# Kernel tuning notes

Measured on AMD Instinct MI355X. Metric: run time of the kernel, lower is better.

## Reference

```python
import jax, jax.numpy as jnp
import numpy as np

H = 512      # hidden_dim
K = 3        # conv_kernel_size
CHUNK = 3    # chunk_size
EPS = 1e-5   # BatchNorm eps


def conv1d(x, w, b, pad):
    # x: (B, Cin, L), w: (Cout, Cin, K)
    y = jax.lax.conv_general_dilated(x, w, (1,), [(pad, pad)],
                                     dimension_numbers=("NCH", "OIH", "NCH"))
    return y + b[None, :, None]


def chunk_indices(seq_lens):
    # static int metadata -> numpy index build (loop over small fixed batch only)
    sl = np.asarray(seq_lens)
    bidx, sidx = [], []
    for b, l in enumerate(sl):
        starts = np.arange(0, int(l) - CHUNK + 1, CHUNK)
        bidx.append(np.full(starts.shape[0], b, dtype=np.int32))
        sidx.append(starts.astype(np.int32))
    return np.concatenate(bidx), np.concatenate(sidx)


def setup_inputs() -> dict:
    key = jax.random.key(0)
    ks = jax.random.split(key, 8)
    B, L = 32, 4096
    x = jax.random.normal(ks[0], (B, L), jnp.float32)
    seq_lens = jax.random.randint(ks[1], (B,), 2048, L + 1)

    def w(k, shape):
        return jax.random.normal(k, shape, jnp.float32) * 0.05

    return {
        "x": x,
        "w0": w(ks[2], (H, 1, K)), "b0": jnp.zeros((H,)), "g0": jnp.ones((H,)), "be0": jnp.zeros((H,)),
        "w1": w(ks[3], (H, H, K)), "b1": jnp.zeros((H,)), "g1": jnp.ones((H,)), "be1": jnp.zeros((H,)),
        "w2": w(ks[4], (H, H, K)), "b2": jnp.zeros((H,)), "g2": jnp.ones((H,)), "be2": jnp.zeros((H,)),
        "pw": w(ks[5], (H, H, CHUNK)), "pb": jnp.zeros((H,)),
        "fw": w(ks[6], (1, H)), "fb": jnp.zeros((1,)),
        "seq_lens": seq_lens,
    }


def reference(x, w0, b0, g0, be0, w1, b1, g1, be1, w2, b2, g2, be2,
              pw, pb, fw, fb, seq_lens):
    inv = np.float32(1.0 / np.sqrt(1.0 + EPS))  # BN eval: mean=0, var=1
    h = x[:, None, :]  # (B, 1, L)
    for (w, b, g, be) in ((w0, b0, g0, be0), (w1, b1, g1, be1), (w2, b2, g2, be2)):
        h = jax.nn.relu(conv1d(h, w, b, pad=1))
        h = (g * inv)[None, :, None] * h + be[None, :, None]
    h = jnp.transpose(h, (0, 2, 1))  # (B, L, H)

    bidx_np, sidx_np = chunk_indices(seq_lens)
    bidx = jnp.asarray(bidx_np)
    sidx = jnp.asarray(sidx_np)
    offs = jnp.arange(CHUNK, dtype=jnp.int32)
    chunks = h[bidx[:, None], sidx[:, None] + offs[None, :], :]  # (N, CHUNK, H)

    # pre_fc_conv over a length-CHUNK window == one GEMM per chunk
    z = jnp.einsum("nth,cht->nc", chunks, pw) + pb  # (N, H)
    logits = jax.nn.relu(z) @ fw.T + fb             # (N, 1)
    return jax.nn.sigmoid(logits)[:, 0]             # (N,)
```

## Files before the change

kernel.cpp:

```cpp
#include <hip/hip_runtime.h>

#define HCH 512
#define LSEQ 4096
#define HSTR (LSEQ + 4)
#define NB 32
#define KW 3
#define KDIM 1536
#define INVS 0.9999950000374997f
#define NT 24

typedef __attribute__((ext_vector_type(8))) short bf16x8;
typedef __attribute__((ext_vector_type(4))) float f32x4;

__device__ inline unsigned short f2bf(float f) {
  unsigned int u = __float_as_uint(f);
  u += 0x7fffu + ((u >> 16) & 1u);
  return (unsigned short)(u >> 16);
}

__device__ inline void gl_lds16(const void* g, void* l) {
  __builtin_amdgcn_global_load_lds(
      (const __attribute__((address_space(1))) void*)g,
      (__attribute__((address_space(3))) void*)l, 16, 0, 0);
}

__global__ void prep_all(const float* __restrict__ w1, const float* __restrict__ w2,
                         const float* __restrict__ pw, unsigned short* __restrict__ wt,
                         const int* __restrict__ seq_lens, int* __restrict__ cum,
                         float* __restrict__ pz, int nz,
                         unsigned short* __restrict__ hbuf, int nbp) {
  int idx = blockIdx.x * 256 + threadIdx.x;
  if (idx < nz) pz[idx] = 0.f;
  if (idx == 0) {
    int acc = 0;
    for (int b = 0; b < NB; b++) {
      cum[b] = acc;
      acc += (seq_lens[b] - KW) / KW + 1;
    }
  }
  int npads = 2 * nbp * 4 * HCH;
  if (idx < npads) {
    int per = nbp * 4 * HCH;
    int buf = idx / per, r = idx % per;
    int b = r / (4 * HCH), rr = r % (4 * HCH);
    int j = rr / HCH, c = rr % HCH;
    int row = (j == 0) ? 0 : (LSEQ + j);
    hbuf[((size_t)buf * nbp + b) * HSTR * HCH + (size_t)row * HCH + c] = 0;
  }
  if (idx < 3 * HCH * KDIM) {
    int which = idx / (HCH * KDIM);
    int r = idx % (HCH * KDIM);
    int c = r / KDIM;
    int rem = r % KDIM;
    int k = rem / HCH, ci = rem % HCH;
    const float* src = (which == 0) ? w1 : ((which == 1) ? w2 : pw);
    wt[idx] = f2bf(src[c * KDIM + ci * KW + k]);
  }
}

__global__ void layer0(const float* __restrict__ x, const float* __restrict__ w0,
                       const float* __restrict__ b0, const float* __restrict__ g0,
                       const float* __restrict__ be0, unsigned short* __restrict__ h0,
                       const int* __restrict__ seq_q) {
  int tid = threadIdx.x;
  int wave = tid >> 6, lane = tid & 63;
  int pos0 = (blockIdx.x * 4 + wave) * 8;
  int l0 = pos0 & (LSEQ - 1);
  int bq = pos0 >> 12;
  if (l0 >= seq_q[bq] + 2) return;
  int c0 = lane * 8;

  float w[24], bb[8], gg[8], ee[8];
  for (int v = 0; v < 6; v++)
    *reinterpret_cast<float4*>(w + v * 4) = *reinterpret_cast<const float4*>(w0 + c0 * 3 + v * 4);
  for (int v = 0; v < 2; v++) {
    *reinterpret_cast<float4*>(bb + v * 4) = *reinterpret_cast<const float4*>(b0 + c0 + v * 4);
    *reinterpret_cast<float4*>(gg + v * 4) = *reinterpret_cast<const float4*>(g0 + c0 + v * 4);
    *reinterpret_cast<float4*>(ee + v * 4) = *reinterpret_cast<const float4*>(be0 + c0 + v * 4);
  }
  for (int c = 0; c < 8; c++) gg[c] *= INVS;

  const float* xb = x + (size_t)(pos0 - l0);
  unsigned short* hrow = h0 + ((size_t)bq * HSTR + 1 + l0) * HCH + c0;
  for (int pp = 0; pp < 8; pp++) {
    int l = l0 + pp;
    float xm1 = (l > 0) ? xb[l - 1] : 0.f;
    float xc = xb[l];
    float xp1 = (l < LSEQ - 1) ? xb[l + 1] : 0.f;
    unsigned int o[4];
    for (int pq = 0; pq < 4; pq++) {
      unsigned int lo = 0, hi = 0;
      for (int s = 0; s < 2; s++) {
        int c = pq * 2 + s;
        float y = w[c * 3] * xm1 + w[c * 3 + 1] * xc + w[c * 3 + 2] * xp1 + bb[c];
        y = fmaxf(y, 0.f);
        unsigned int u = f2bf(gg[c] * y + ee[c]);
        if (s == 0) lo = u; else hi = u;
      }
      o[pq] = lo | (hi << 16);
    }
    uint4 v4; v4.x = o[0]; v4.y = o[1]; v4.z = o[2]; v4.w = o[3];
    *reinterpret_cast<uint4*>(hrow + (size_t)pp * HCH) = v4;
  }
}

#define OFFK(T) (((T) % 3) * HCH + ((T) / 3) * 64)

#define STAGE_A(Mh, AB, TN)                                                 \
  { char* d_ = ldsc + (AB) * 32768 + (Mh) * 16384 + w * 1024;               \
    gl_lds16(aSrc[Mh][0] + OFFK(TN), d_);                                   \
    gl_lds16(aSrc[Mh][1] + OFFK(TN), d_ + 8192); }

#define STAGE_B(Nh, BB, TN)                                                 \
  { char* d_ = ldsc + 65536 + (BB) * 32768 + (Nh) * 16384 + w * 1024;       \
    gl_lds16(bSrc[Nh][0] + OFFK(TN), d_);                                   \
    gl_lds16(bSrc[Nh][1] + OFFK(TN), d_ + 8192); }

#define LOAD_AF(Mh, AB)                                                     \
  _Pragma("unroll") for (int i_ = 0; i_ < 4; ++i_)                          \
  _Pragma("unroll") for (int s_ = 0; s_ < 2; ++s_)                          \
    af[i_][s_] = *reinterpret_cast<const bf16x8*>(                          \
        ldsb + (AB) * 16384 + (Mh) * 8192 + (wm + i_ * 16 + mr) * 64 +      \
        (((s_ * 4 + quad) ^ (mr & 7)) << 3));

#define LOAD_BF(Nh, BB)                                                     \
  _Pragma("unroll") for (int j_ = 0; j_ < 2; ++j_)                          \
  _Pragma("unroll") for (int s_ = 0; s_ < 2; ++s_)                          \
    bfv[Nh][j_][s_] = *reinterpret_cast<const bf16x8*>(                     \
        ldsb + 32768 + (BB) * 16384 + (Nh) * 8192 + (wn + j_ * 16 + mr) * 64 + \
        (((s_ * 4 + quad) ^ (mr & 7)) << 3));

#define MFMA_Q(MB, Nh)                                                      \
  __builtin_amdgcn_s_setprio(1);                                            \
  _Pragma("unroll") for (int i_ = 0; i_ < 4; ++i_)                          \
  _Pragma("unroll") for (int j_ = 0; j_ < 2; ++j_)                          \
  _Pragma("unroll") for (int s_ = 0; s_ < 2; ++s_)                          \
    acc[(MB) + i_][(Nh)*2 + j_] = __builtin_amdgcn_mfma_f32_16x16x32_bf16(  \
        af[i_][s_], bfv[Nh][j_][s_], acc[(MB) + i_][(Nh)*2 + j_], 0, 0, 0); \
  __builtin_amdgcn_s_setprio(0);

#define BARRIER { asm volatile("" ::: "memory");                            \
                  __builtin_amdgcn_s_barrier();                             \
                  asm volatile("" ::: "memory"); }
#define WAITV(n) asm volatile("s_waitcnt vmcnt(" #n ")" ::: "memory");

#define STEP(T)                                                             \
  {                                                                         \
    if ((T) == NT - 1) { WAITV(0); } else { WAITV(4); }                     \
    BARRIER;                                                                \
    if ((T) + 1 < NT) { STAGE_A(0, ((T)+1)&1, (T)+1);                       \
                        STAGE_A(1, ((T)+1)&1, (T)+1); }                     \
    if ((T) + 2 < NT) { STAGE_B(0, ((T)+2)%3, (T)+2);                       \
                        STAGE_B(1, ((T)+2)%3, (T)+2); }                     \
    bf16x8 af[4][2], bfv[2][2][2];                                          \
    LOAD_AF(0, (T)&1);                                                      \
    LOAD_BF(0, (T)%3); LOAD_BF(1, (T)%3);                                   \
    MFMA_Q(0, 0); MFMA_Q(0, 1);                                             \
    LOAD_AF(1, (T)&1);                                                      \
    MFMA_Q(4, 1); MFMA_Q(4, 0);                                             \
  }

__global__ __launch_bounds__(512, 2) void conv_gemm8(
    const unsigned short* __restrict__ hin,
    const unsigned short* __restrict__ wT,
    const float* __restrict__ bconv, const float* __restrict__ g,
    const float* __restrict__ be,
    unsigned short* __restrict__ hout,
    const int* __restrict__ seq_q, int margin) {
  __shared__ unsigned short ldsb[81920];

  int f = blockIdx.x;
  int cpx = gridDim.x >> 3;
  int s = (f & 7) * cpx + (f >> 3);
  int cm = (s & 1) << 8;
  int y = s >> 1;
  int b = y >> 4;
  int l0 = (y & 15) << 8;
  int limit = seq_q[b] + margin;
  if (l0 >= limit) return;

  const size_t hb = (size_t)b * HSTR * HCH + HCH;
  int tid = threadIdx.x;
  int w = tid >> 6, lane = tid & 63;
  int quad = lane >> 4, mr = lane & 15;
  int wm = (w >> 2) << 6;
  int wn = (w & 3) << 5;
  int srow = tid >> 3;
  int sslot8 = (((tid & 7) ^ (srow & 7)) << 3);

  const unsigned short* aSrc[2][2];
#pragma unroll
  for (int Mh = 0; Mh < 2; ++Mh)
#pragma unroll
    for (int g2 = 0; g2 < 2; ++g2)
      aSrc[Mh][g2] = wT + (size_t)(cm + Mh * 128 + g2 * 64 + srow) * KDIM + sslot8;
  const unsigned short* bSrc[2][2];
#pragma unroll
  for (int Nh = 0; Nh < 2; ++Nh)
#pragma unroll
    for (int g2 = 0; g2 < 2; ++g2)
      bSrc[Nh][g2] = hin + hb +
          (size_t)(l0 - 1 + Nh * 128 + g2 * 64 + srow) * HCH + sslot8;

  f32x4 acc[8][4] = {};
  char* ldsc = (char*)ldsb;

  STAGE_A(0, 0, 0); STAGE_A(1, 0, 0);
  STAGE_B(0, 0, 0); STAGE_B(1, 0, 0);
  STAGE_B(0, 1, 1); STAGE_B(1, 1, 1);

  STEP(0)  STEP(1)  STEP(2)  STEP(3)  STEP(4)  STEP(5)
  STEP(6)  STEP(7)  STEP(8)  STEP(9)  STEP(10) STEP(11)
  STEP(12) STEP(13) STEP(14) STEP(15) STEP(16) STEP(17)
  STEP(18) STEP(19) STEP(20) STEP(21) STEP(22) STEP(23)

#pragma unroll
  for (int ai = 0; ai < 8; ++ai) {
    int Mh = ai >> 2, i = ai & 3;
    int c = cm + Mh * 128 + wm + i * 16 + quad * 4;
    f32x4 bc = *reinterpret_cast<const f32x4*>(bconv + c);
    f32x4 gg = *reinterpret_cast<const f32x4*>(g + c);
    f32x4 bb = *reinterpret_cast<const f32x4*>(be + c);
#pragma unroll
    for (int aj = 0; aj < 4; ++aj) {
      int Nh = aj >> 1, j = aj & 1;
      int n = l0 + Nh * 128 + wn + j * 16 + (lane & 15);
      if (n >= limit) continue;
      unsigned long long pack = 0;
#pragma unroll
      for (int r = 0; r < 4; ++r) {
        float yv = acc[ai][aj][r] + bc[r];
        yv = fmaxf(yv, 0.f);
        unsigned long long u = f2bf(gg[r] * INVS * yv + bb[r]);
        pack |= u << (16 * r);
      }
      *reinterpret_cast<unsigned long long*>(hout + hb + (size_t)n * HCH + c) = pack;
    }
  }
}

__global__ __launch_bounds__(512, 2) void chunk_gemm8(
    const unsigned short* __restrict__ h2,
    const unsigned short* __restrict__ wT,
    const float* __restrict__ pb, const float* __restrict__ fw,
    const int* __restrict__ seq_q,
    const int* __restrict__ cum_q,
    float* __restrict__ partial,
    const unsigned short* __restrict__ zp) {
  __shared__ unsigned short ldsb[81920];

  int f = blockIdx.x;
  int cpx = gridDim.x >> 3;
  int s = (f & 7) * cpx + (f >> 3);
  int cm = (s & 1) << 8;
  int y = s >> 1;
  int b = y / 6;
  int s_base = (y % 6) << 8;
  int slen = seq_q[b];
  if (3 * s_base + KW > slen) return;

  const size_t hb = (size_t)b * HSTR * HCH + HCH;
  int tid = threadIdx.x;
  int w = tid >> 6, lane = tid & 63;
  int quad = lane >> 4, mr = lane & 15;
  int wm = (w >> 2) << 6;
  int wn = (w & 3) << 5;
  int srow = tid >> 3;
  int sslot8 = (((tid & 7) ^ (srow & 7)) << 3);

  const unsigned short* aSrc[2][2];
#pragma unroll
  for (int Mh = 0; Mh < 2; ++Mh)
#pragma unroll
    for (int g2 = 0; g2 < 2; ++g2)
      aSrc[Mh][g2] = wT + (size_t)(cm + Mh * 128 + g2 * 64 + srow) * KDIM + sslot8;
  const unsigned short* bSrc[2][2];
#pragma unroll
  for (int Nh = 0; Nh < 2; ++Nh)
#pragma unroll
    for (int g2 = 0; g2 < 2; ++g2) {
      int slot = s_base + Nh * 128 + g2 * 64 + srow;
      bSrc[Nh][g2] = (slot <= 1365)
          ? h2 + hb + (size_t)(3 * slot) * HCH + sslot8
          : zp + sslot8;
    }

  f32x4 acc[8][4] = {};
  char* ldsc = (char*)ldsb;

  STAGE_A(0, 0, 0); STAGE_A(1, 0, 0);
  STAGE_B(0, 0, 0); STAGE_B(1, 0, 0);
  STAGE_B(0, 1, 1); STAGE_B(1, 1, 1);

  STEP(0)  STEP(1)  STEP(2)  STEP(3)  STEP(4)  STEP(5)
  STEP(6)  STEP(7)  STEP(8)  STEP(9)  STEP(10) STEP(11)
  STEP(12) STEP(13) STEP(14) STEP(15) STEP(16) STEP(17)
  STEP(18) STEP(19) STEP(20) STEP(21) STEP(22) STEP(23)

  int nn = lane & 15;
#pragma unroll
  for (int aj = 0; aj < 4; ++aj) {
    int Nh = aj >> 1, jj = aj & 1;
    int sc = s_base + Nh * 128 + wn + jj * 16 + nn;
    float sacc = 0.f;
#pragma unroll
    for (int ai = 0; ai < 8; ++ai) {
      int Mh = ai >> 2, i = ai & 3;
      int c = cm + Mh * 128 + wm + i * 16 + quad * 4;
      f32x4 pbv = *reinterpret_cast<const f32x4*>(pb + c);
      f32x4 fwv = *reinterpret_cast<const f32x4*>(fw + c);
#pragma unroll
      for (int r = 0; r < 4; ++r) {
        float z = acc[ai][aj][r] + pbv[r];
        z = fmaxf(z, 0.f);
        sacc += z * fwv[r];
      }
    }
    sacc += __shfl_xor(sacc, 16, 64);
    sacc += __shfl_xor(sacc, 32, 64);
    if (quad == 0 && 3 * sc + KW <= slen)
      atomicAdd(partial + cum_q[b] + sc, sacc);
  }
}

__global__ void finalize(const float* __restrict__ partial, const float* __restrict__ fb,
                         float* __restrict__ out, int n) {
  int i = blockIdx.x * 256 + threadIdx.x;
  if (i < n) {
    float t = partial[i] + fb[0];
    out[i] = 1.f / (1.f + expf(-t));
  }
}

extern "C" void kernel_launch(void* const* d_in, const int* in_sizes, int n_in,
                              void* d_out, int out_size, void* d_ws, size_t ws_size,
                              hipStream_t stream) {
  (void)in_sizes; (void)n_in;
  const float* x   = (const float*)d_in[0];
  const float* w0  = (const float*)d_in[1];
  const float* b0  = (const float*)d_in[2];
  const float* g0  = (const float*)d_in[3];
  const float* be0 = (const float*)d_in[4];
  const float* w1  = (const float*)d_in[5];
  const float* b1  = (const float*)d_in[6];
  const float* g1  = (const float*)d_in[7];
  const float* be1 = (const float*)d_in[8];
  const float* w2  = (const float*)d_in[9];
  const float* b2  = (const float*)d_in[10];
  const float* g2  = (const float*)d_in[11];
  const float* be2 = (const float*)d_in[12];
  const float* pw  = (const float*)d_in[13];
  const float* pb  = (const float*)d_in[14];
  const float* fw  = (const float*)d_in[15];
  const float* fb  = (const float*)d_in[16];
  const int* seq_lens = (const int*)d_in[17];

  char* ws = (char*)d_ws;
  unsigned short* zeropage = (unsigned short*)ws;
  float* partial = (float*)(ws + 4096);
  size_t off = 4096 + (size_t)out_size * 4;
  off = (off + 255) & ~(size_t)255;
  int* cum = (int*)(ws + off);
  off += NB * 4;
  off = (off + 255) & ~(size_t)255;
  unsigned short* wt = (unsigned short*)(ws + off);
  off += (size_t)3 * HCH * KDIM * 2;
  off = (off + 255) & ~(size_t)255;
  size_t fixed = off;

  const size_t per_batch = (size_t)HSTR * HCH * 2;
  int nb_pass = NB;
  while (nb_pass > 1 && fixed + 2 * per_batch * (size_t)nb_pass > ws_size)
    nb_pass >>= 1;
  unsigned short* h0 = (unsigned short*)(ws + fixed);
  unsigned short* h1 = h0 + (size_t)nb_pass * HSTR * HCH;

  int nzero = 1024 + out_size;
  prep_all<<<(3 * HCH * KDIM) / 256, 256, 0, stream>>>(w1, w2, pw, wt, seq_lens, cum,
                                                       (float*)ws, nzero, h0, nb_pass);

  int npass = NB / nb_pass;
  for (int q = 0; q < npass; q++) {
    const float* xq = x + (size_t)q * nb_pass * LSEQ;
    const int* sq = seq_lens + q * nb_pass;
    int nwg = nb_pass * 32;
    layer0<<<nb_pass * (LSEQ / 32), 256, 0, stream>>>(xq, w0, b0, g0, be0, h0, sq);
    conv_gemm8<<<nwg, 512, 0, stream>>>(h0, wt, b1, g1, be1, h1, sq, 1);
    conv_gemm8<<<nwg, 512, 0, stream>>>(h1, wt + (size_t)HCH * KDIM, b2, g2, be2, h0,
                                        sq, 0);
    int nwg2 = nb_pass * 12;
    chunk_gemm8<<<nwg2, 512, 0, stream>>>(h0, wt + (size_t)2 * HCH * KDIM, pb, fw,
                                          sq, cum + q * nb_pass, partial, zeropage);
  }
  finalize<<<(out_size + 255) / 256, 256, 0, stream>>>(partial, fb, (float*)d_out, out_size);
}
```

Measured before the change: 556.4 us.

## Reuse one staged activation window across the three conv taps

The conv GEMM now stages a single 320-row activation window (258 rows used, the rest padded from a zero page) per 64-channel slice into LDS. It reads all three tap offsets from that window by shifting the row index, where before it reloaded shifted B tiles for each tap. This cuts global-to-LDS traffic for the activation operand to roughly a third. In exchange the pipeline is reshaped: B staging is spread over three steps with double buffering by channel slice, and the vmcnt waits change, which may expose load latency at slice boundaries.

```diff
diff --git a/kernel.cpp b/kernel.cpp
--- a/kernel.cpp
+++ b/kernel.cpp
@@ -104,30 +104,23 @@
   }
 }
 
+#define BARRIER { asm volatile("" ::: "memory");                            \
+                  __builtin_amdgcn_s_barrier();                             \
+                  asm volatile("" ::: "memory"); }
+#define WAITV(n) asm volatile("s_waitcnt vmcnt(" #n ")" ::: "memory");
+
 #define OFFK(T) (((T) % 3) * HCH + ((T) / 3) * 64)
 
 #define STAGE_A(Mh, AB, TN)                                                 \
   { char* d_ = ldsc + (AB) * 32768 + (Mh) * 16384 + w * 1024;               \
     gl_lds16(aSrc[Mh][0] + OFFK(TN), d_);                                   \
     gl_lds16(aSrc[Mh][1] + OFFK(TN), d_ + 8192); }
-
-#define STAGE_B(Nh, BB, TN)                                                 \
-  { char* d_ = ldsc + 65536 + (BB) * 32768 + (Nh) * 16384 + w * 1024;       \
-    gl_lds16(bSrc[Nh][0] + OFFK(TN), d_);                                   \
-    gl_lds16(bSrc[Nh][1] + OFFK(TN), d_ + 8192); }
 
 #define LOAD_AF(Mh, AB)                                                     \
   _Pragma("unroll") for (int i_ = 0; i_ < 4; ++i_)                          \
   _Pragma("unroll") for (int s_ = 0; s_ < 2; ++s_)                          \
     af[i_][s_] = *reinterpret_cast<const bf16x8*>(                          \
         ldsb + (AB) * 16384 + (Mh) * 8192 + (wm + i_ * 16 + mr) * 64 +      \
-        (((s_ * 4 + quad) ^ (mr & 7)) << 3));
-
-#define LOAD_BF(Nh, BB)                                                     \
-  _Pragma("unroll") for (int j_ = 0; j_ < 2; ++j_)                          \
-  _Pragma("unroll") for (int s_ = 0; s_ < 2; ++s_)                          \
-    bfv[Nh][j_][s_] = *reinterpret_cast<const bf16x8*>(                     \
-        ldsb + 32768 + (BB) * 16384 + (Nh) * 8192 + (wn + j_ * 16 + mr) * 64 + \
         (((s_ * 4 + quad) ^ (mr & 7)) << 3));
 
 #define MFMA_Q(MB, Nh)                                                      \
@@ -139,10 +132,128 @@
         af[i_][s_], bfv[Nh][j_][s_], acc[(MB) + i_][(Nh)*2 + j_], 0, 0, 0); \
   __builtin_amdgcn_s_setprio(0);
 
-#define BARRIER { asm volatile("" ::: "memory");                            \
-                  __builtin_amdgcn_s_barrier();                             \
-                  asm volatile("" ::: "memory"); }
-#define WAITV(n) asm volatile("s_waitcnt vmcnt(" #n ")" ::: "memory");
+#define STAGE_BS(PB, S)                                                     \
+  gl_lds16(bSw[S] + (PB) * 64,                                              \
+           ldsc + 65536 + ((PB) & 1) * 40960 + (S) * 8192 + w * 1024);
+
+#define LOAD_BFD(Nh, CB, K)                                                 \
+  _Pragma("unroll") for (int j_ = 0; j_ < 2; ++j_)                          \
+  _Pragma("unroll") for (int s_ = 0; s_ < 2; ++s_) {                        \
+    int r_ = (Nh) * 128 + wn + j_ * 16 + mr + (K);                          \
+    bfv[Nh][j_][s_] = *reinterpret_cast<const bf16x8*>(                     \
+        ldsb + 32768 + (CB) * 20480 + r_ * 64 +                             \
+        (((s_ * 4 + quad) ^ (r_ & 7)) << 3)); }
+
+#define STEPD(T)                                                            \
+  {                                                                         \
+    if ((T) % 3 == 0 || (T) >= 21) { WAITV(0); } else { WAITV(2); }         \
+    BARRIER;                                                                \
+    if ((T) + 1 < NT) { STAGE_A(0, ((T)+1)&1, (T)+1);                       \
+                        STAGE_A(1, ((T)+1)&1, (T)+1); }                     \
+    if ((T) / 3 + 1 < 8) {                                                  \
+      if ((T) % 3 == 0) { STAGE_BS((T)/3 + 1, 0); STAGE_BS((T)/3 + 1, 1); } \
+      if ((T) % 3 == 1) { STAGE_BS((T)/3 + 1, 2); STAGE_BS((T)/3 + 1, 3); } \
+      if ((T) % 3 == 2) { STAGE_BS((T)/3 + 1, 4); }                         \
+    }                                                                       \
+    bf16x8 af[4][2], bfv[2][2][2];                                          \
+    LOAD_AF(0, (T)&1);                                                      \
+    LOAD_BFD(0, ((T)/3)&1, (T)%3); LOAD_BFD(1, ((T)/3)&1, (T)%3);           \
+    MFMA_Q(0, 0); MFMA_Q(0, 1);                                             \
+    LOAD_AF(1, (T)&1);                                                      \
+    MFMA_Q(4, 1); MFMA_Q(4, 0);                                             \
+  }
+
+__global__ __launch_bounds__(512, 2) void conv_gemmd(
+    const unsigned short* __restrict__ hin,
+    const unsigned short* __restrict__ wT,
+    const float* __restrict__ bconv, const float* __restrict__ g,
+    const float* __restrict__ be,
+    unsigned short* __restrict__ hout,
+    const unsigned short* __restrict__ zp,
+    const int* __restrict__ seq_q, int margin) {
+  __shared__ unsigned short ldsb[73728];
+
+  int f = blockIdx.x;
+  int cpx = gridDim.x >> 3;
+  int s = (f & 7) * cpx + (f >> 3);
+  int cm = (s & 1) << 8;
+  int y = s >> 1;
+  int b = y >> 4;
+  int l0 = (y & 15) << 8;
+  int limit = seq_q[b] + margin;
+  if (l0 >= limit) return;
+
+  const size_t hb = (size_t)b * HSTR * HCH + HCH;
+  int tid = threadIdx.x;
+  int w = tid >> 6, lane = tid & 63;
+  int quad = lane >> 4, mr = lane & 15;
+  int wm = (w >> 2) << 6;
+  int wn = (w & 3) << 5;
+  int srow = tid >> 3;
+  int sslot8 = (((tid & 7) ^ (srow & 7)) << 3);
+
+  const unsigned short* aSrc[2][2];
+#pragma unroll
+  for (int Mh = 0; Mh < 2; ++Mh)
+#pragma unroll
+    for (int g2 = 0; g2 < 2; ++g2)
+      aSrc[Mh][g2] = wT + (size_t)(cm + Mh * 128 + g2 * 64 + srow) * KDIM + sslot8;
+
+  const unsigned short* bSw[5];
+#pragma unroll
+  for (int sw = 0; sw < 5; ++sw) {
+    int r = sw * 64 + srow;
+    bSw[sw] = (r <= 258) ? hin + hb + (size_t)(l0 - 1 + r) * HCH + sslot8
+                         : zp + sslot8;
+  }
+
+  f32x4 acc[8][4] = {};
+  char* ldsc = (char*)ldsb;
+
+  STAGE_A(0, 0, 0); STAGE_A(1, 0, 0);
+  STAGE_BS(0, 0); STAGE_BS(0, 1); STAGE_BS(0, 2); STAGE_BS(0, 3); STAGE_BS(0, 4);
+
+  STEPD(0)  STEPD(1)  STEPD(2)  STEPD(3)  STEPD(4)  STEPD(5)
+  STEPD(6)  STEPD(7)  STEPD(8)  STEPD(9)  STEPD(10) STEPD(11)
+  STEPD(12) STEPD(13) STEPD(14) STEPD(15) STEPD(16) STEPD(17)
+  STEPD(18) STEPD(19) STEPD(20) STEPD(21) STEPD(22) STEPD(23)
+
+#pragma unroll
+  for (int ai = 0; ai < 8; ++ai) {
+    int Mh = ai >> 2, i = ai & 3;
+    int c = cm + Mh * 128 + wm + i * 16 + quad * 4;
+    f32x4 bc = *reinterpret_cast<const f32x4*>(bconv + c);
+    f32x4 gg = *reinterpret_cast<const f32x4*>(g + c);
+    f32x4 bb = *reinterpret_cast<const f32x4*>(be + c);
+#pragma unroll
+    for (int aj = 0; aj < 4; ++aj) {
+      int Nh = aj >> 1, j = aj & 1;
+      int n = l0 + Nh * 128 + wn + j * 16 + (lane & 15);
+      if (n >= limit) continue;
+      unsigned long long pack = 0;
+#pragma unroll
+      for (int r = 0; r < 4; ++r) {
+        float yv = acc[ai][aj][r] + bc[r];
+        yv = fmaxf(yv, 0.f);
+        unsigned long long u = f2bf(gg[r] * INVS * yv + bb[r]);
+        pack |= u << (16 * r);
+      }
+      *reinterpret_cast<unsigned long long*>(hout + hb + (size_t)n * HCH + c) = pack;
+    }
+  }
+}
+
+#define STAGE_B(Nh, BB, TN)                                                 \
+  { char* d_ = ldsc + 65536 + (BB) * 32768 + (Nh) * 16384 + w * 1024;       \
+    gl_lds16(bSrc[Nh][0] + OFFK(TN), d_);                                   \
+    gl_lds16(bSrc[Nh][1] + OFFK(TN), d_ + 8192); }
+
+#define LOAD_BF(Nh, BB)                                                     \
+  _Pragma("unroll") for (int j_ = 0; j_ < 2; ++j_)                          \
+  _Pragma("unroll") for (int s_ = 0; s_ < 2; ++s_)                          \
+    bfv[Nh][j_][s_] = *reinterpret_cast<const bf16x8*>(                     \
+        ldsb + 32768 + (BB) * 16384 + (Nh) * 8192 + (wn + j_ * 16 + mr) * 64 + \
+        (((s_ * 4 + quad) ^ (mr & 7)) << 3));
 
 #define STEP(T)                                                             \
   {                                                                         \
@@ -159,85 +270,6 @@
     LOAD_AF(1, (T)&1);                                                      \
     MFMA_Q(4, 1); MFMA_Q(4, 0);                                             \
   }
-
-__global__ __launch_bounds__(512, 2) void conv_gemm8(
-    const unsigned short* __restrict__ hin,
-    const unsigned short* __restrict__ wT,
-    const float* __restrict__ bconv, const float* __restrict__ g,
-    const float* __restrict__ be,
-    unsigned short* __restrict__ hout,
-    const int* __restrict__ seq_q, int margin) {
-  __shared__ unsigned short ldsb[81920];
-
-  int f = blockIdx.x;
-  int cpx = gridDim.x >> 3;
-  int s = (f & 7) * cpx + (f >> 3);
-  int cm = (s & 1) << 8;
-  int y = s >> 1;
-  int b = y >> 4;
-  int l0 = (y & 15) << 8;
-  int limit = seq_q[b] + margin;
-  if (l0 >= limit) return;
-
-  const size_t hb = (size_t)b * HSTR * HCH + HCH;
-  int tid = threadIdx.x;
-  int w = tid >> 6, lane = tid & 63;
-  int quad = lane >> 4, mr = lane & 15;
-  int wm = (w >> 2) << 6;
-  int wn = (w & 3) << 5;
-  int srow = tid >> 3;
-  int sslot8 = (((tid & 7) ^ (srow & 7)) << 3);
-
-  const unsigned short* aSrc[2][2];
-#pragma unroll
-  for (int Mh = 0; Mh < 2; ++Mh)
-#pragma unroll
-    for (int g2 = 0; g2 < 2; ++g2)
-      aSrc[Mh][g2] = wT + (size_t)(cm + Mh * 128 + g2 * 64 + srow) * KDIM + sslot8;
-  const unsigned short* bSrc[2][2];
-#pragma unroll
-  for (int Nh = 0; Nh < 2; ++Nh)
-#pragma unroll
-    for (int g2 = 0; g2 < 2; ++g2)
-      bSrc[Nh][g2] = hin + hb +
-          (size_t)(l0 - 1 + Nh * 128 + g2 * 64 + srow) * HCH + sslot8;
-
-  f32x4 acc[8][4] = {};
-  char* ldsc = (char*)ldsb;
-
-  STAGE_A(0, 0, 0); STAGE_A(1, 0, 0);
-  STAGE_B(0, 0, 0); STAGE_B(1, 0, 0);
-  STAGE_B(0, 1, 1); STAGE_B(1, 1, 1);
-
-  STEP(0)  STEP(1)  STEP(2)  STEP(3)  STEP(4)  STEP(5)
-  STEP(6)  STEP(7)  STEP(8)  STEP(9)  STEP(10) STEP(11)
-  STEP(12) STEP(13) STEP(14) STEP(15) STEP(16) STEP(17)
-  STEP(18) STEP(19) STEP(20) STEP(21) STEP(22) STEP(23)
-
-#pragma unroll
-  for (int ai = 0; ai < 8; ++ai) {
-    int Mh = ai >> 2, i = ai & 3;
-    int c = cm + Mh * 128 + wm + i * 16 + quad * 4;
-    f32x4 bc = *reinterpret_cast<const f32x4*>(bconv + c);
-    f32x4 gg = *reinterpret_cast<const f32x4*>(g + c);
-    f32x4 bb = *reinterpret_cast<const f32x4*>(be + c);
-#pragma unroll
-    for (int aj = 0; aj < 4; ++aj) {
-      int Nh = aj >> 1, j = aj & 1;
-      int n = l0 + Nh * 128 + wn + j * 16 + (lane & 15);
-      if (n >= limit) continue;
-      unsigned long long pack = 0;
-#pragma unroll
-      for (int r = 0; r < 4; ++r) {
-        float yv = acc[ai][aj][r] + bc[r];
-        yv = fmaxf(yv, 0.f);
-        unsigned long long u = f2bf(gg[r] * INVS * yv + bb[r]);
-        pack |= u << (16 * r);
-      }
-      *reinterpret_cast<unsigned long long*>(hout + hb + (size_t)n * HCH + c) = pack;
-    }
-  }
-}
 
 __global__ __launch_bounds__(512, 2) void chunk_gemm8(
     const unsigned short* __restrict__ h2,
@@ -385,9 +417,9 @@
     const int* sq = seq_lens + q * nb_pass;
     int nwg = nb_pass * 32;
     layer0<<<nb_pass * (LSEQ / 32), 256, 0, stream>>>(xq, w0, b0, g0, be0, h0, sq);
-    conv_gemm8<<<nwg, 512, 0, stream>>>(h0, wt, b1, g1, be1, h1, sq, 1);
-    conv_gemm8<<<nwg, 512, 0, stream>>>(h1, wt + (size_t)HCH * KDIM, b2, g2, be2, h0,
-                                        sq, 0);
+    conv_gemmd<<<nwg, 512, 0, stream>>>(h0, wt, b1, g1, be1, h1, zeropage, sq, 1);
+    conv_gemmd<<<nwg, 512, 0, stream>>>(h1, wt + (size_t)HCH * KDIM, b2, g2, be2, h0,
+                                        zeropage, sq, 0);
     int nwg2 = nb_pass * 12;
     chunk_gemm8<<<nwg2, 512, 0, stream>>>(h0, wt + (size_t)2 * HCH * KDIM, pb, fw,
                                           sq, cum + q * nb_pass, partial, zeropage);
```

Measured after the change: 563.5 us. About the same (+1.3%).

## Load weight fragments directly from global memory in conv GEMM, stage only activations

Applied to the files above, without the earlier changes.

Replaces the conv-layer GEMM with a variant that reads the A (weight) MFMA fragments straight from global memory into registers instead of staging them through LDS. Only the activation tile is staged via global_load_lds into a triple buffer, which shrinks LDS from 160KB to 96KB per block, and the barrier and wait placement is reordered. The goal is to cut LDS traffic and staging instructions and ease occupancy limits. The cost is that weight loads now go through the cache with strided per-lane access and their latency sits on the MFMA critical path.

```diff
diff --git a/kernel.cpp b/kernel.cpp
--- a/kernel.cpp
+++ b/kernel.cpp
@@ -104,31 +104,12 @@
   }
 }
 
+#define BARRIER { asm volatile("" ::: "memory");                            \
+                  __builtin_amdgcn_s_barrier();                             \
+                  asm volatile("" ::: "memory"); }
+#define WAITV(n) asm volatile("s_waitcnt vmcnt(" #n ")" ::: "memory");
+
 #define OFFK(T) (((T) % 3) * HCH + ((T) / 3) * 64)
-
-#define STAGE_A(Mh, AB, TN)                                                 \
-  { char* d_ = ldsc + (AB) * 32768 + (Mh) * 16384 + w * 1024;               \
-    gl_lds16(aSrc[Mh][0] + OFFK(TN), d_);                                   \
-    gl_lds16(aSrc[Mh][1] + OFFK(TN), d_ + 8192); }
-
-#define STAGE_B(Nh, BB, TN)                                                 \
-  { char* d_ = ldsc + 65536 + (BB) * 32768 + (Nh) * 16384 + w * 1024;       \
-    gl_lds16(bSrc[Nh][0] + OFFK(TN), d_);                                   \
-    gl_lds16(bSrc[Nh][1] + OFFK(TN), d_ + 8192); }
-
-#define LOAD_AF(Mh, AB)                                                     \
-  _Pragma("unroll") for (int i_ = 0; i_ < 4; ++i_)                          \
-  _Pragma("unroll") for (int s_ = 0; s_ < 2; ++s_)                          \
-    af[i_][s_] = *reinterpret_cast<const bf16x8*>(                          \
-        ldsb + (AB) * 16384 + (Mh) * 8192 + (wm + i_ * 16 + mr) * 64 +      \
-        (((s_ * 4 + quad) ^ (mr & 7)) << 3));
-
-#define LOAD_BF(Nh, BB)                                                     \
-  _Pragma("unroll") for (int j_ = 0; j_ < 2; ++j_)                          \
-  _Pragma("unroll") for (int s_ = 0; s_ < 2; ++s_)                          \
-    bfv[Nh][j_][s_] = *reinterpret_cast<const bf16x8*>(                     \
-        ldsb + 32768 + (BB) * 16384 + (Nh) * 8192 + (wn + j_ * 16 + mr) * 64 + \
-        (((s_ * 4 + quad) ^ (mr & 7)) << 3));
 
 #define MFMA_Q(MB, Nh)                                                      \
   __builtin_amdgcn_s_setprio(1);                                            \
@@ -139,10 +120,141 @@
         af[i_][s_], bfv[Nh][j_][s_], acc[(MB) + i_][(Nh)*2 + j_], 0, 0, 0); \
   __builtin_amdgcn_s_setprio(0);
 
-#define BARRIER { asm volatile("" ::: "memory");                            \
-                  __builtin_amdgcn_s_barrier();                             \
-                  asm volatile("" ::: "memory"); }
-#define WAITV(n) asm volatile("s_waitcnt vmcnt(" #n ")" ::: "memory");
+#define LOAD_AG(Mh, T)                                                      \
+  _Pragma("unroll") for (int i_ = 0; i_ < 4; ++i_)                          \
+  _Pragma("unroll") for (int s_ = 0; s_ < 2; ++s_)                          \
+    af[i_][s_] = *reinterpret_cast<const bf16x8*>(                          \
+        aP[Mh][i_] + OFFK(T) + s_ * 32);
+
+#define STAGE_B2(Nh, BB, TN)                                                \
+  { char* d_ = ldsc + (BB) * 32768 + (Nh) * 16384 + w * 1024;               \
+    gl_lds16(bSrc[Nh][0] + OFFK(TN), d_);                                   \
+    gl_lds16(bSrc[Nh][1] + OFFK(TN), d_ + 8192); }
+
+#define LOAD_BF2(Nh, BB)                                                    \
+  _Pragma("unroll") for (int j_ = 0; j_ < 2; ++j_)                          \
+  _Pragma("unroll") for (int s_ = 0; s_ < 2; ++s_)                          \
+    bfv[Nh][j_][s_] = *reinterpret_cast<const bf16x8*>(                     \
+        ldsb + (BB) * 16384 + (Nh) * 8192 + (wn + j_ * 16 + mr) * 64 +      \
+        (((s_ * 4 + quad) ^ (mr & 7)) << 3));
+
+#define STEPL(T)                                                            \
+  {                                                                         \
+    BARRIER;                                                                \
+    bf16x8 af[4][2], bfv[2][2][2];                                          \
+    LOAD_AG(0, T);                                                          \
+    LOAD_BF2(0, (T) % 3); LOAD_BF2(1, (T) % 3);                             \
+    MFMA_Q(0, 0); MFMA_Q(0, 1);                                             \
+    LOAD_AG(1, T);                                                          \
+    if ((T) + 2 < NT) { STAGE_B2(0, ((T)+2)%3, (T)+2);                      \
+                        STAGE_B2(1, ((T)+2)%3, (T)+2); }                    \
+    MFMA_Q(4, 1); MFMA_Q(4, 0);                                             \
+    if ((T) + 2 < NT) { WAITV(4); } else { WAITV(0); }                      \
+  }
+
+__global__ __launch_bounds__(512, 2) void conv_gemmA(
+    const unsigned short* __restrict__ hin,
+    const unsigned short* __restrict__ wT,
+    const float* __restrict__ bconv, const float* __restrict__ g,
+    const float* __restrict__ be,
+    unsigned short* __restrict__ hout,
+    const int* __restrict__ seq_q, int margin) {
+  __shared__ unsigned short ldsb[49152];
+
+  int f = blockIdx.x;
+  int cpx = gridDim.x >> 3;
+  int s = (f & 7) * cpx + (f >> 3);
+  int cm = (s & 1) << 8;
+  int y = s >> 1;
+  int b = y >> 4;
+  int l0 = (y & 15) << 8;
+  int limit = seq_q[b] + margin;
+  if (l0 >= limit) return;
+
+  const size_t hb = (size_t)b * HSTR * HCH + HCH;
+  int tid = threadIdx.x;
+  int w = tid >> 6, lane = tid & 63;
+  int quad = lane >> 4, mr = lane & 15;
+  int wm = (w >> 2) << 6;
+  int wn = (w & 3) << 5;
+  int srow = tid >> 3;
+  int sslot8 = (((tid & 7) ^ (srow & 7)) << 3);
+
+  const unsigned short* aP[2][4];
+#pragma unroll
+  for (int Mh = 0; Mh < 2; ++Mh)
+#pragma unroll
+    for (int i = 0; i < 4; ++i)
+      aP[Mh][i] = wT + (size_t)(cm + Mh * 128 + wm + i * 16 + mr) * KDIM + quad * 8;
+
+  const unsigned short* bSrc[2][2];
+#pragma unroll
+  for (int Nh = 0; Nh < 2; ++Nh)
+#pragma unroll
+    for (int g2 = 0; g2 < 2; ++g2)
+      bSrc[Nh][g2] = hin + hb +
+          (size_t)(l0 - 1 + Nh * 128 + g2 * 64 + srow) * HCH + sslot8;
+
+  f32x4 acc[8][4] = {};
+  char* ldsc = (char*)ldsb;
+
+  STAGE_B2(0, 0, 0); STAGE_B2(1, 0, 0);
+  WAITV(0);
+  STAGE_B2(0, 1, 1); STAGE_B2(1, 1, 1);
+
+  STEPL(0)  STEPL(1)  STEPL(2)  STEPL(3)  STEPL(4)  STEPL(5)
+  STEPL(6)  STEPL(7)  STEPL(8)  STEPL(9)  STEPL(10) STEPL(11)
+  STEPL(12) STEPL(13) STEPL(14) STEPL(15) STEPL(16) STEPL(17)
+  STEPL(18) STEPL(19) STEPL(20) STEPL(21) STEPL(22) STEPL(23)
+
+#pragma unroll
+  for (int ai = 0; ai < 8; ++ai) {
+    int Mh = ai >> 2, i = ai & 3;
+    int c = cm + Mh * 128 + wm + i * 16 + quad * 4;
+    f32x4 bc = *reinterpret_cast<const f32x4*>(bconv + c);
+    f32x4 gg = *reinterpret_cast<const f32x4*>(g + c);
+    f32x4 bb = *reinterpret_cast<const f32x4*>(be + c);
+#pragma unroll
+    for (int aj = 0; aj < 4; ++aj) {
+      int Nh = aj >> 1, j = aj & 1;
+      int n = l0 + Nh * 128 + wn + j * 16 + (lane & 15);
+      if (n >= limit) continue;
+      unsigned long long pack = 0;
+#pragma unroll
+      for (int r = 0; r < 4; ++r) {
+        float yv = acc[ai][aj][r] + bc[r];
+        yv = fmaxf(yv, 0.f);
+        unsigned long long u = f2bf(gg[r] * INVS * yv + bb[r]);
+        pack |= u << (16 * r);
+      }
+      *reinterpret_cast<unsigned long long*>(hout + hb + (size_t)n * HCH + c) = pack;
+    }
+  }
+}
+
+#define STAGE_A(Mh, AB, TN)                                                 \
+  { char* d_ = ldsc + (AB) * 32768 + (Mh) * 16384 + w * 1024;               \
+    gl_lds16(aSrc[Mh][0] + OFFK(TN), d_);                                   \
+    gl_lds16(aSrc[Mh][1] + OFFK(TN), d_ + 8192); }
+
+#define STAGE_B(Nh, BB, TN)                                                 \
+  { char* d_ = ldsc + 65536 + (BB) * 32768 + (Nh) * 16384 + w * 1024;       \
+    gl_lds16(bSrc[Nh][0] + OFFK(TN), d_);                                   \
+    gl_lds16(bSrc[Nh][1] + OFFK(TN), d_ + 8192); }
+
+#define LOAD_AF(Mh, AB)                                                     \
+  _Pragma("unroll") for (int i_ = 0; i_ < 4; ++i_)                          \
+  _Pragma("unroll") for (int s_ = 0; s_ < 2; ++s_)                          \
+    af[i_][s_] = *reinterpret_cast<const bf16x8*>(                          \
+        ldsb + (AB) * 16384 + (Mh) * 8192 + (wm + i_ * 16 + mr) * 64 +      \
+        (((s_ * 4 + quad) ^ (mr & 7)) << 3));
+
+#define LOAD_BF(Nh, BB)                                                     \
+  _Pragma("unroll") for (int j_ = 0; j_ < 2; ++j_)                          \
+  _Pragma("unroll") for (int s_ = 0; s_ < 2; ++s_)                          \
+    bfv[Nh][j_][s_] = *reinterpret_cast<const bf16x8*>(                     \
+        ldsb + 32768 + (BB) * 16384 + (Nh) * 8192 + (wn + j_ * 16 + mr) * 64 + \
+        (((s_ * 4 + quad) ^ (mr & 7)) << 3));
 
 #define STEP(T)                                                             \
   {                                                                         \
@@ -159,85 +271,6 @@
     LOAD_AF(1, (T)&1);                                                      \
     MFMA_Q(4, 1); MFMA_Q(4, 0);                                             \
   }
-
-__global__ __launch_bounds__(512, 2) void conv_gemm8(
-    const unsigned short* __restrict__ hin,
-    const unsigned short* __restrict__ wT,
-    const float* __restrict__ bconv, const float* __restrict__ g,
-    const float* __restrict__ be,
-    unsigned short* __restrict__ hout,
-    const int* __restrict__ seq_q, int margin) {
-  __shared__ unsigned short ldsb[81920];
-
-  int f = blockIdx.x;
-  int cpx = gridDim.x >> 3;
-  int s = (f & 7) * cpx + (f >> 3);
-  int cm = (s & 1) << 8;
-  int y = s >> 1;
-  int b = y >> 4;
-  int l0 = (y & 15) << 8;
-  int limit = seq_q[b] + margin;
-  if (l0 >= limit) return;
-
-  const size_t hb = (size_t)b * HSTR * HCH + HCH;
-  int tid = threadIdx.x;
-  int w = tid >> 6, lane = tid & 63;
-  int quad = lane >> 4, mr = lane & 15;
-  int wm = (w >> 2) << 6;
-  int wn = (w & 3) << 5;
-  int srow = tid >> 3;
-  int sslot8 = (((tid & 7) ^ (srow & 7)) << 3);
-
-  const unsigned short* aSrc[2][2];
-#pragma unroll
-  for (int Mh = 0; Mh < 2; ++Mh)
-#pragma unroll
-    for (int g2 = 0; g2 < 2; ++g2)
-      aSrc[Mh][g2] = wT + (size_t)(cm + Mh * 128 + g2 * 64 + srow) * KDIM + sslot8;
-  const unsigned short* bSrc[2][2];
-#pragma unroll
-  for (int Nh = 0; Nh < 2; ++Nh)
-#pragma unroll
-    for (int g2 = 0; g2 < 2; ++g2)
-      bSrc[Nh][g2] = hin + hb +
-          (size_t)(l0 - 1 + Nh * 128 + g2 * 64 + srow) * HCH + sslot8;
-
-  f32x4 acc[8][4] = {};
-  char* ldsc = (char*)ldsb;
-
-  STAGE_A(0, 0, 0); STAGE_A(1, 0, 0);
-  STAGE_B(0, 0, 0); STAGE_B(1, 0, 0);
-  STAGE_B(0, 1, 1); STAGE_B(1, 1, 1);
-
-  STEP(0)  STEP(1)  STEP(2)  STEP(3)  STEP(4)  STEP(5)
-  STEP(6)  STEP(7)  STEP(8)  STEP(9)  STEP(10) STEP(11)
-  STEP(12) STEP(13) STEP(14) STEP(15) STEP(16) STEP(17)
-  STEP(18) STEP(19) STEP(20) STEP(21) STEP(22) STEP(23)
-
-#pragma unroll
-  for (int ai = 0; ai < 8; ++ai) {
-    int Mh = ai >> 2, i = ai & 3;
-    int c = cm + Mh * 128 + wm + i * 16 + quad * 4;
-    f32x4 bc = *reinterpret_cast<const f32x4*>(bconv + c);
-    f32x4 gg = *reinterpret_cast<const f32x4*>(g + c);
-    f32x4 bb = *reinterpret_cast<const f32x4*>(be + c);
-#pragma unroll
-    for (int aj = 0; aj < 4; ++aj) {
-      int Nh = aj >> 1, j = aj & 1;
-      int n = l0 + Nh * 128 + wn + j * 16 + (lane & 15);
-      if (n >= limit) continue;
-      unsigned long long pack = 0;
-#pragma unroll
-      for (int r = 0; r < 4; ++r) {
-        float yv = acc[ai][aj][r] + bc[r];
-        yv = fmaxf(yv, 0.f);
-        unsigned long long u = f2bf(gg[r] * INVS * yv + bb[r]);
-        pack |= u << (16 * r);
-      }
-      *reinterpret_cast<unsigned long long*>(hout + hb + (size_t)n * HCH + c) = pack;
-    }
-  }
-}
 
 __global__ __launch_bounds__(512, 2) void chunk_gemm8(
     const unsigned short* __restrict__ h2,
@@ -385,8 +418,8 @@
     const int* sq = seq_lens + q * nb_pass;
     int nwg = nb_pass * 32;
     layer0<<<nb_pass * (LSEQ / 32), 256, 0, stream>>>(xq, w0, b0, g0, be0, h0, sq);
-    conv_gemm8<<<nwg, 512, 0, stream>>>(h0, wt, b1, g1, be1, h1, sq, 1);
-    conv_gemm8<<<nwg, 512, 0, stream>>>(h1, wt + (size_t)HCH * KDIM, b2, g2, be2, h0,
+    conv_gemmA<<<nwg, 512, 0, stream>>>(h0, wt, b1, g1, be1, h1, sq, 1);
+    conv_gemmA<<<nwg, 512, 0, stream>>>(h1, wt + (size_t)HCH * KDIM, b2, g2, be2, h0,
                                         sq, 0);
     int nwg2 = nb_pass * 12;
     chunk_gemm8<<<nwg2, 512, 0, stream>>>(h0, wt + (size_t)2 * HCH * KDIM, pb, fw,
```

Result: slower. 1.118 ms (+101.0%).
